# Optimization experiments

Hardware: AMD Instinct MI355X
Metric: run time of the kernel (lower is better)

Reference implementation:

```python
import jax, jax.numpy as jnp
import numpy as np

N, E = 10000, 320000
IN_D, HID, OUT_D, EIN, KH = 128, 32, 128, 1, 32
BN_EPS = 1e-5  # torch BatchNorm1d default eps


def bn(x, g, b):
    # training-mode batch norm with biased variance (torch normalization semantics)
    m = jnp.mean(x, axis=0)
    v = jnp.mean((x - m) ** 2, axis=0)
    return g * (x - m) / jnp.sqrt(v + BN_EPS) + b


def setup_inputs() -> dict:
    key = jax.random.key(0)
    ks = jax.random.split(key, 8)

    def w(k, shape, s=0.05):
        return jax.random.normal(k, shape, dtype=jnp.float32) * s

    return {
        "H": jax.random.normal(ks[0], (N, IN_D), dtype=jnp.float32),
        "edge_attr": jax.random.normal(ks[1], (E, EIN), dtype=jnp.float32),
        "edges": jax.random.randint(ks[2], (2, E), 0, N),
        # linear1: input_dim -> hidden_dim
        "w1": w(ks[3], (HID, IN_D)), "b1": jnp.zeros((HID,), jnp.float32),
        # kernel MLP: edge_input_dim -> kernel_hidden -> (hidden+1)*hidden
        "kw1": w(ks[4], (KH, EIN)), "kb1": jnp.zeros((KH,), jnp.float32),
        "kw2": w(ks[5], ((HID + 1) * HID, KH)), "kb2": jnp.zeros(((HID + 1) * HID,), jnp.float32),
        # linear2: hidden -> output
        "w2": w(ks[6], (OUT_D, HID)), "b2": jnp.zeros((OUT_D,), jnp.float32),
        # batchnorm affine params
        "g_in": jnp.ones((IN_D,), jnp.float32), "beta_in": jnp.zeros((IN_D,), jnp.float32),
        "g_msg": jnp.ones((HID,), jnp.float32), "beta_msg": jnp.zeros((HID,), jnp.float32),
        "g_upd": jnp.ones((HID,), jnp.float32), "beta_upd": jnp.zeros((HID,), jnp.float32),
        "g_out": jnp.ones((OUT_D,), jnp.float32), "beta_out": jnp.zeros((OUT_D,), jnp.float32),
    }


def reference(H, edge_attr, edges, w1, b1, kw1, kb1, kw2, kb2, w2, b2,
              g_in, beta_in, g_msg, beta_msg, g_upd, beta_upd, g_out, beta_out):
    node_out, node_in = edges[0], edges[1]

    Hn = bn(H, g_in, beta_in)                    # input_batch_norm
    layer_input = jax.nn.relu(Hn)                # dropout -> identity (eval)

    # message: gather -> linear1 -> BN -> relu
    msg = layer_input[node_in] @ w1.T + b1       # [E, HID]
    msg = jax.nn.relu(bn(msg, g_msg, beta_msg))

    # edge-conditioned dynamic kernel: [E, HID+1, HID]
    kern = jax.nn.relu(edge_attr @ kw1.T + kb1) @ kw2.T + kb2
    kern = kern.reshape(E, HID + 1, HID)
    # per-edge matvec + per-edge bias row
    msg = jnp.einsum('ejk,ek->ej', kern[:, 1:, :], msg) + kern[:, 0, :]

    # aggregate: scatter_add into nodes
    upd = jax.ops.segment_sum(msg, node_out, num_segments=N)
    upd = jax.nn.relu(bn(upd, g_upd, beta_upd))

    out = upd @ w2.T + b2                        # linear2
    return bn(out, g_out, beta_out)              # output_batch_norm
```

## Files before the change

### kernel.cpp

```cpp
#include <hip/hip_runtime.h>
#include <math.h>

constexpr int N_    = 10000;
constexpr int E_    = 320000;
constexpr int IND   = 128;
constexpr int HID   = 32;
constexpr int OUTD  = 128;
constexpr int NIV   = 33;
constexpr float EPS = 1e-5f;

constexpr size_t OFF_SUMH = 0;
constexpr size_t OFF_SQH  = 128;
constexpr size_t OFF_SUMP = 256;
constexpr size_t OFF_SQP  = 288;
constexpr size_t OFF_SUMU = 320;
constexpr size_t OFF_SQU  = 352;
constexpr size_t OFF_SUMO = 384;
constexpr size_t OFF_SQO  = 512;
constexpr size_t OFF_OCC  = 640;
constexpr size_t OFF_DEG  = 704;
constexpr size_t OFF_UPD  = 10752;
constexpr size_t ZERO_CNT = OFF_UPD + (size_t)N_*HID;
constexpr size_t OFF_BPS  = ZERO_CNT;
constexpr size_t OFF_M    = OFF_BPS + 32;
constexpr size_t OFF_C1   = 330816;
constexpr size_t OFF_C0   = OFF_C1 + (size_t)NIV*1056;
constexpr size_t OFF_P    = OFF_C0 + (size_t)NIV*1056;
constexpr size_t OFF_Q    = OFF_P + (size_t)N_*HID;
constexpr size_t OFF_IDX  = OFF_Q + (size_t)N_*HID;
constexpr size_t OFF_Y    = OFF_IDX + (size_t)E_;

__global__ __launch_bounds__(128)
void k_intervals(const float* __restrict__ kw1, const float* __restrict__ kb1,
                 const float* __restrict__ kw2, const float* __restrict__ kb2,
                 float* __restrict__ ws) {
    __shared__ float sel1[32], sel0[32];
    int* wsi = (int*)ws;
    int i = blockIdx.x;
    if (threadIdx.x == 0) {
        float bp[32]; int m = 0;
        for (int t = 0; t < 32; ++t) {
            float w = kw1[t];
            if (w != 0.f) bp[m++] = -kb1[t] / w;
        }
        for (int a = 1; a < m; ++a) {
            float v = bp[a]; int b = a - 1;
            while (b >= 0 && bp[b] > v) { bp[b+1] = bp[b]; --b; }
            bp[b+1] = v;
        }
        if (i == 0) {
            for (int k = 0; k < 32; ++k) ws[OFF_BPS + k] = (k < m) ? bp[k] : 0.f;
            wsi[OFF_M] = m;
        }
        float arep;
        if (m == 0 || i > m) arep = 0.f;
        else if (i == 0)     arep = bp[0]   - (1.f + 0.5f*fabsf(bp[0]));
        else if (i == m)     arep = bp[m-1] + (1.f + 0.5f*fabsf(bp[m-1]));
        else                 arep = (bp[i-1] < bp[i]) ? 0.5f*(bp[i-1] + bp[i]) : bp[i-1];
        for (int t = 0; t < 32; ++t) {
            bool s = (arep * kw1[t] + kb1[t]) > 0.f;
            sel1[t] = s ? kw1[t] : 0.f;
            sel0[t] = s ? kb1[t] : 0.f;
        }
    }
    __syncthreads();
    for (int r = threadIdx.x; r < 1056; r += blockDim.x) {
        float a1 = 0.f, a0 = 0.f;
        for (int t = 0; t < 32; ++t) {
            float w = kw2[r*32 + t];
            a1 += w * sel1[t];
            a0 += w * sel0[t];
        }
        ws[OFF_C1 + (size_t)i*1056 + r] = a1;
        ws[OFF_C0 + (size_t)i*1056 + r] = a0 + kb2[r];
    }
}

__global__ __launch_bounds__(256)
void k_stats_H(const float* __restrict__ H, float* __restrict__ ws) {
    __shared__ float shS[256], shQ[256];
    int t = threadIdx.x;
    int col = t & 127, half = t >> 7;
    float s = 0.f, q = 0.f;
    for (int r = blockIdx.x*2 + half; r < N_; r += gridDim.x*2) {
        float x = H[(size_t)r*IND + col];
        s += x; q += x*x;
    }
    shS[t] = s; shQ[t] = q;
    __syncthreads();
    if (t < 128) {
        atomicAdd(&ws[OFF_SUMH + t], shS[t] + shS[t+128]);
        atomicAdd(&ws[OFF_SQH  + t], shQ[t] + shQ[t+128]);
    }
}

__global__ __launch_bounds__(256)
void k_edge_idx(const float* __restrict__ ea, const int* __restrict__ edges,
                float* __restrict__ ws) {
    __shared__ int locc[NIV];
    __shared__ float bps[32];
    __shared__ int sm;
    int* wsi = (int*)ws;
    int t = threadIdx.x;
    if (t < NIV) locc[t] = 0;
    if (t < 32)  bps[t] = ws[OFF_BPS + t];
    if (t == 0)  sm = wsi[OFF_M];
    __syncthreads();
    int m = sm;
    for (int e = blockIdx.x*blockDim.x + t; e < E_; e += gridDim.x*blockDim.x) {
        float a = ea[e];
        int cnt = 0;
        for (int k = 0; k < m; ++k) cnt += (bps[k] < a) ? 1 : 0;
        wsi[OFF_IDX + e] = cnt;
        atomicAdd(&locc[cnt], 1);
        atomicAdd(&wsi[OFF_DEG + edges[E_ + e]], 1);
    }
    __syncthreads();
    if (t < NIV && locc[t] > 0) atomicAdd(&wsi[OFF_OCC + t], locc[t]);
}

__global__ __launch_bounds__(256)
void k_nodeP(const float* __restrict__ H, const float* __restrict__ w1,
             const float* __restrict__ b1, const float* __restrict__ g_in,
             const float* __restrict__ beta_in, float* __restrict__ ws) {
    __shared__ float X[2][IND];
    __shared__ float shP[256];
    int t = threadIdx.x;
    int nh = t >> 7, c = t & 127;
    float mean = ws[OFF_SUMH + c] * (1.f/N_);
    float var  = ws[OFF_SQH  + c] * (1.f/N_) - mean*mean;
    float istd = 1.f / sqrtf(var + EPS);
    float gc = g_in[c] * istd, bc = beta_in[c] - mean * gc;
    int j = c & 31, qd = c >> 5;
    for (int base = blockIdx.x*2; base < N_; base += gridDim.x*2) {
        int n = base + nh;
        float x = H[(size_t)n*IND + c];
        X[nh][c] = fmaxf(gc*x + bc, 0.f);
        __syncthreads();
        float part = 0.f;
        const float* wrow = w1 + j*IND + qd*32;
        const float* xq   = &X[nh][qd*32];
        for (int k = 0; k < 32; ++k) part += wrow[k] * xq[k];
        shP[t] = part;
        __syncthreads();
        if (c < 32) {
            float p = shP[nh*128 + j] + shP[nh*128 + j + 32]
                    + shP[nh*128 + j + 64] + shP[nh*128 + j + 96] + b1[j];
            ws[OFF_P + (size_t)n*HID + j] = p;
        }
        __syncthreads();
    }
}

__global__ __launch_bounds__(256)
void k_msg_stats(float* __restrict__ ws) {
    __shared__ float shS[256], shQ[256];
    const int* wsi = (const int*)ws;
    int t = threadIdx.x, j = t & 31, cp = t >> 5;
    float s = 0.f, q = 0.f;
    for (int n = blockIdx.x*8 + cp; n < N_; n += gridDim.x*8) {
        float w = (float)wsi[OFF_DEG + n];
        float p = ws[OFF_P + (size_t)n*HID + j];
        s += w*p; q += w*p*p;
    }
    shS[t] = s; shQ[t] = q;
    __syncthreads();
    if (t < 32) {
        float S = 0.f, Qq = 0.f;
        for (int c = 0; c < 8; ++c) { S += shS[t + 32*c]; Qq += shQ[t + 32*c]; }
        atomicAdd(&ws[OFF_SUMP + t], S);
        atomicAdd(&ws[OFF_SQP  + t], Qq);
    }
}

__global__ __launch_bounds__(256)
void k_Qy(const float* __restrict__ g_msg, const float* __restrict__ beta_msg,
          float* __restrict__ ws, int max_slots) {
    __shared__ float QL[8][HID];
    __shared__ int inv_slot[NIV];
    __shared__ int nslot;
    const int* wsi = (const int*)ws;
    int t = threadIdx.x, ln = t >> 5, j = t & 31;
    if (t == 0) {
        int ns = 0;
        for (int i = 0; i < NIV; ++i)
            if (wsi[OFF_OCC + i] > 0 && ns < max_slots) inv_slot[ns++] = i;
        nslot = ns;
    }
    __syncthreads();
    int ns = nslot;
    float mP = ws[OFF_SUMP + j] * (1.f/E_);
    float vP = ws[OFF_SQP  + j] * (1.f/E_) - mP*mP;
    float istd = 1.f / sqrtf(vP + EPS);
    float gc = g_msg[j]*istd, bc = beta_msg[j] - mP*gc;
    float2* yy = (float2*)(ws + OFF_Y);
    for (int base = blockIdx.x*8; base < N_; base += gridDim.x*8) {
        int n = base + ln;
        float p = ws[OFF_P + (size_t)n*HID + j];
        float qv = fmaxf(gc*p + bc, 0.f);
        ws[OFF_Q + (size_t)n*HID + j] = qv;
        QL[ln][j] = qv;
        __syncthreads();
        for (int s = 0; s < ns; ++s) {
            int i = inv_slot[s];
            const float* C1r = ws + OFF_C1 + (size_t)i*1056;
            const float* C0r = ws + OFF_C0 + (size_t)i*1056;
            float a1 = 0.f, a0 = 0.f;
            const float* ql = QL[ln];
            for (int k = 0; k < 32; ++k) {
                float qk = ql[k];
                a1 += C1r[32 + j*32 + k] * qk;
                a0 += C0r[32 + j*32 + k] * qk;
            }
            yy[((size_t)s*N_ + n)*32 + j] = make_float2(a1 + C1r[j], a0 + C0r[j]);
        }
        __syncthreads();
    }
}

__global__ __launch_bounds__(256)
void k_edge(const float* __restrict__ ea, const int* __restrict__ edges,
            float* __restrict__ ws, int max_slots) {
    __shared__ int slotL[NIV];
    const int* wsi = (const int*)ws;
    int t = threadIdx.x;
    if (t == 0) {
        int ns = 0;
        for (int i = 0; i < NIV; ++i) {
            if (wsi[OFF_OCC + i] > 0 && ns < max_slots) slotL[i] = ns++;
            else slotL[i] = -1;
        }
    }
    __syncthreads();
    long long g = (long long)blockIdx.x*blockDim.x + t;
    if (g >= (long long)E_*32) return;
    int e = (int)(g >> 5), j = (int)(g & 31);
    float a = ea[e];
    int i   = wsi[OFF_IDX + e];
    int s   = slotL[i];
    int nin = edges[E_ + e], nout = edges[e];
    float r;
    if (s >= 0) {
        const float2* yy = (const float2*)(ws + OFF_Y);
        float2 v = yy[((size_t)s*N_ + nin)*32 + j];
        r = fmaf(a, v.x, v.y);
    } else {
        const float* C1r = ws + OFF_C1 + (size_t)i*1056;
        const float* C0r = ws + OFF_C0 + (size_t)i*1056;
        const float* Qn  = ws + OFF_Q + (size_t)nin*HID;
        float a1 = 0.f, a0 = 0.f;
        for (int k = 0; k < 32; ++k) {
            float qk = Qn[k];
            a1 += C1r[32 + j*32 + k] * qk;
            a0 += C0r[32 + j*32 + k] * qk;
        }
        r = a*(a1 + C1r[j]) + (a0 + C0r[j]);
    }
    atomicAdd(&ws[OFF_UPD + (size_t)nout*HID + j], r);
}

__global__ __launch_bounds__(256)
void k_upd_stats(float* __restrict__ ws) {
    __shared__ float shS[256], shQ[256];
    int t = threadIdx.x, j = t & 31, cp = t >> 5;
    float s = 0.f, q = 0.f;
    for (int n = blockIdx.x*8 + cp; n < N_; n += gridDim.x*8) {
        float u = ws[OFF_UPD + (size_t)n*HID + j];
        s += u; q += u*u;
    }
    shS[t] = s; shQ[t] = q;
    __syncthreads();
    if (t < 32) {
        float S = 0.f, Qq = 0.f;
        for (int c = 0; c < 8; ++c) { S += shS[t + 32*c]; Qq += shQ[t + 32*c]; }
        atomicAdd(&ws[OFF_SUMU + t], S);
        atomicAdd(&ws[OFF_SQU  + t], Qq);
    }
}

__global__ __launch_bounds__(256)
void k_out(const float* __restrict__ w2, const float* __restrict__ b2,
           const float* __restrict__ g_upd, const float* __restrict__ beta_upd,
           float* __restrict__ ws, float* __restrict__ out) {
    __shared__ float U[2][HID];
    __shared__ float shS[256], shQ[256];
    int t = threadIdx.x, nh = t >> 7, o = t & 127;
    float gc = 0.f, bc = 0.f;
    if (o < 32) {
        float m = ws[OFF_SUMU + o]*(1.f/N_);
        float v = ws[OFF_SQU  + o]*(1.f/N_) - m*m;
        float istd = 1.f/sqrtf(v + EPS);
        gc = g_upd[o]*istd; bc = beta_upd[o] - m*gc;
    }
    float w2r[32];
    for (int k = 0; k < 32; ++k) w2r[k] = w2[o*32 + k];
    float bo = b2[o];
    float sO = 0.f, qO = 0.f;
    for (int base = blockIdx.x*2; base < N_; base += gridDim.x*2) {
        int n = base + nh;
        if (o < 32) {
            float u = ws[OFF_UPD + (size_t)n*HID + o];
            U[nh][o] = fmaxf(gc*u + bc, 0.f);
        }
        __syncthreads();
        float v = bo;
        for (int k = 0; k < 32; ++k) v += w2r[k]*U[nh][k];
        out[(size_t)n*OUTD + o] = v;
        sO += v; qO += v*v;
        __syncthreads();
    }
    shS[t] = sO; shQ[t] = qO;
    __syncthreads();
    if (t < 128) {
        atomicAdd(&ws[OFF_SUMO + t], shS[t] + shS[t+128]);
        atomicAdd(&ws[OFF_SQO  + t], shQ[t] + shQ[t+128]);
    }
}

__global__ __launch_bounds__(256)
void k_norm(const float* __restrict__ g_out, const float* __restrict__ beta_out,
            const float* __restrict__ ws, float* __restrict__ out) {
    int g = blockIdx.x*blockDim.x + threadIdx.x;
    if (g >= N_*OUTD) return;
    int o = g & 127;
    float m = ws[OFF_SUMO + o]*(1.f/N_);
    float v = ws[OFF_SQO  + o]*(1.f/N_) - m*m;
    float istd = 1.f/sqrtf(v + EPS);
    out[g] = g_out[o]*istd*(out[g] - m) + beta_out[o];
}

extern "C" void kernel_launch(void* const* d_in, const int* in_sizes, int n_in,
                              void* d_out, int out_size, void* d_ws, size_t ws_size,
                              hipStream_t stream) {
    const float* H        = (const float*)d_in[0];
    const float* ea       = (const float*)d_in[1];
    const int*   edges    = (const int*)  d_in[2];
    const float* w1       = (const float*)d_in[3];
    const float* b1       = (const float*)d_in[4];
    const float* kw1      = (const float*)d_in[5];
    const float* kb1      = (const float*)d_in[6];
    const float* kw2      = (const float*)d_in[7];
    const float* kb2      = (const float*)d_in[8];
    const float* w2       = (const float*)d_in[9];
    const float* b2       = (const float*)d_in[10];
    const float* g_in     = (const float*)d_in[11];
    const float* beta_in  = (const float*)d_in[12];
    const float* g_msg    = (const float*)d_in[13];
    const float* beta_msg = (const float*)d_in[14];
    const float* g_upd    = (const float*)d_in[15];
    const float* beta_upd = (const float*)d_in[16];
    const float* g_out    = (const float*)d_in[17];
    const float* beta_out = (const float*)d_in[18];
    float* ws  = (float*)d_ws;
    float* out = (float*)d_out;

    int max_slots = 0;
    size_t avail = ws_size / 4;
    if (avail > OFF_Y) max_slots = (int)((avail - OFF_Y) / ((size_t)N_*2*HID));
    if (max_slots > NIV) max_slots = NIV;

    hipMemsetAsync(d_ws, 0, ZERO_CNT*sizeof(float), stream);
    hipLaunchKernelGGL(k_intervals, dim3(NIV), dim3(128), 0, stream, kw1, kb1, kw2, kb2, ws);
    hipLaunchKernelGGL(k_stats_H,  dim3(128),  dim3(256), 0, stream, H, ws);
    hipLaunchKernelGGL(k_edge_idx, dim3(313),  dim3(256), 0, stream, ea, edges, ws);
    hipLaunchKernelGGL(k_nodeP,    dim3(1250), dim3(256), 0, stream, H, w1, b1, g_in, beta_in, ws);
    hipLaunchKernelGGL(k_msg_stats,dim3(64),   dim3(256), 0, stream, ws);
    hipLaunchKernelGGL(k_Qy,       dim3(1250), dim3(256), 0, stream, g_msg, beta_msg, ws, max_slots);
    hipLaunchKernelGGL(k_edge,     dim3((E_*32)/256), dim3(256), 0, stream, ea, edges, ws, max_slots);
    hipLaunchKernelGGL(k_upd_stats,dim3(64),   dim3(256), 0, stream, ws);
    hipLaunchKernelGGL(k_out,      dim3(250),  dim3(256), 0, stream, w2, b2, g_upd, beta_upd, ws, out);
    hipLaunchKernelGGL(k_norm,     dim3((N_*OUTD+255)/256), dim3(256), 0, stream, g_out, beta_out, ws, out);
}
```

Before: 311.1 us.

## Replace atomic edge scatter with CSR-sorted per-node gather and fused kernels

Builds a CSR by destination node (degree count, prefix scan, atomic slot placement) and computes each node's aggregate with a per-warp gather, replacing the per-element float atomics into the update buffer. For the two most common kernel intervals it accumulates a-weighted and plain sums of the per-edge message vectors and applies the shared 32x32 matrices once per node. Many small kernels are merged into fewer launches with block-range dispatch, and the node projection is rewritten with w1 held in shared memory. The per-node loop is serial over edges and its length varies with degree, which causes load imbalance, and it adds a sort step that itself uses atomics.

```diff
diff --git a/kernel.cpp b/kernel.cpp
--- a/kernel.cpp
+++ b/kernel.cpp
@@ -9,266 +9,307 @@
 constexpr int NIV   = 33;
 constexpr float EPS = 1e-5f;
 
-constexpr size_t OFF_SUMH = 0;
-constexpr size_t OFF_SQH  = 128;
-constexpr size_t OFF_SUMP = 256;
-constexpr size_t OFF_SQP  = 288;
-constexpr size_t OFF_SUMU = 320;
-constexpr size_t OFF_SQU  = 352;
-constexpr size_t OFF_SUMO = 384;
-constexpr size_t OFF_SQO  = 512;
-constexpr size_t OFF_OCC  = 640;
-constexpr size_t OFF_DEG  = 704;
-constexpr size_t OFF_UPD  = 10752;
-constexpr size_t ZERO_CNT = OFF_UPD + (size_t)N_*HID;
-constexpr size_t OFF_BPS  = ZERO_CNT;
-constexpr size_t OFF_M    = OFF_BPS + 32;
-constexpr size_t OFF_C1   = 330816;
-constexpr size_t OFF_C0   = OFF_C1 + (size_t)NIV*1056;
-constexpr size_t OFF_P    = OFF_C0 + (size_t)NIV*1056;
-constexpr size_t OFF_Q    = OFF_P + (size_t)N_*HID;
-constexpr size_t OFF_IDX  = OFF_Q + (size_t)N_*HID;
-constexpr size_t OFF_Y    = OFF_IDX + (size_t)E_;
-
-__global__ __launch_bounds__(128)
-void k_intervals(const float* __restrict__ kw1, const float* __restrict__ kb1,
-                 const float* __restrict__ kw2, const float* __restrict__ kb2,
-                 float* __restrict__ ws) {
+constexpr size_t OFF_SUMH   = 0;
+constexpr size_t OFF_SQH    = 128;
+constexpr size_t OFF_SUMP   = 256;
+constexpr size_t OFF_SQP    = 288;
+constexpr size_t OFF_SUMU   = 320;
+constexpr size_t OFF_SQU    = 352;
+constexpr size_t OFF_SUMO   = 384;
+constexpr size_t OFF_SQO    = 512;
+constexpr size_t OFF_OCC    = 640;
+constexpr size_t OFF_DEGIN  = 704;
+constexpr size_t OFF_DEGOUT = 10704;
+constexpr size_t ZERO_CNT   = 20704;
+constexpr size_t OFF_STARTS = 20740;
+constexpr size_t OFF_CUR    = 30744;
+constexpr size_t OFF_C1     = 40744;
+constexpr size_t OFF_C0     = 75592;
+constexpr size_t OFF_P      = 110440;
+constexpr size_t OFF_UPD    = 430440;
+constexpr size_t OFF_SORT   = 750440;
+constexpr size_t OFF_IDX    = 1070440;
+
+__device__ inline int compute_bps(const float* kw1, const float* kb1, float* bp) {
+    int m = 0;
+    for (int k = 0; k < 32; ++k) {
+        float w = kw1[k];
+        if (w != 0.f) bp[m++] = -kb1[k] / w;
+    }
+    for (int a = 1; a < m; ++a) {
+        float v = bp[a]; int b = a - 1;
+        while (b >= 0 && bp[b] > v) { bp[b+1] = bp[b]; --b; }
+        bp[b+1] = v;
+    }
+    return m;
+}
+
+__global__ __launch_bounds__(256)
+void k_A(const float* __restrict__ H,
+         const float* __restrict__ ea, const int* __restrict__ edges,
+         const float* __restrict__ kw1, const float* __restrict__ kb1,
+         const float* __restrict__ kw2, const float* __restrict__ kb2,
+         float* __restrict__ ws) {
     __shared__ float sel1[32], sel0[32];
-    int* wsi = (int*)ws;
-    int i = blockIdx.x;
-    if (threadIdx.x == 0) {
-        float bp[32]; int m = 0;
-        for (int t = 0; t < 32; ++t) {
-            float w = kw1[t];
-            if (w != 0.f) bp[m++] = -kb1[t] / w;
-        }
-        for (int a = 1; a < m; ++a) {
-            float v = bp[a]; int b = a - 1;
-            while (b >= 0 && bp[b] > v) { bp[b+1] = bp[b]; --b; }
-            bp[b+1] = v;
-        }
-        if (i == 0) {
-            for (int k = 0; k < 32; ++k) ws[OFF_BPS + k] = (k < m) ? bp[k] : 0.f;
-            wsi[OFF_M] = m;
-        }
-        float arep;
-        if (m == 0 || i > m) arep = 0.f;
-        else if (i == 0)     arep = bp[0]   - (1.f + 0.5f*fabsf(bp[0]));
-        else if (i == m)     arep = bp[m-1] + (1.f + 0.5f*fabsf(bp[m-1]));
-        else                 arep = (bp[i-1] < bp[i]) ? 0.5f*(bp[i-1] + bp[i]) : bp[i-1];
-        for (int t = 0; t < 32; ++t) {
-            bool s = (arep * kw1[t] + kb1[t]) > 0.f;
-            sel1[t] = s ? kw1[t] : 0.f;
-            sel0[t] = s ? kb1[t] : 0.f;
-        }
-    }
-    __syncthreads();
-    for (int r = threadIdx.x; r < 1056; r += blockDim.x) {
-        float a1 = 0.f, a0 = 0.f;
-        for (int t = 0; t < 32; ++t) {
-            float w = kw2[r*32 + t];
-            a1 += w * sel1[t];
-            a0 += w * sel0[t];
-        }
-        ws[OFF_C1 + (size_t)i*1056 + r] = a1;
-        ws[OFF_C0 + (size_t)i*1056 + r] = a0 + kb2[r];
-    }
-}
-
-__global__ __launch_bounds__(256)
-void k_stats_H(const float* __restrict__ H, float* __restrict__ ws) {
     __shared__ float shS[256], shQ[256];
-    int t = threadIdx.x;
-    int col = t & 127, half = t >> 7;
-    float s = 0.f, q = 0.f;
-    for (int r = blockIdx.x*2 + half; r < N_; r += gridDim.x*2) {
-        float x = H[(size_t)r*IND + col];
-        s += x; q += x*x;
-    }
-    shS[t] = s; shQ[t] = q;
-    __syncthreads();
-    if (t < 128) {
-        atomicAdd(&ws[OFF_SUMH + t], shS[t] + shS[t+128]);
-        atomicAdd(&ws[OFF_SQH  + t], shQ[t] + shQ[t+128]);
-    }
-}
-
-__global__ __launch_bounds__(256)
-void k_edge_idx(const float* __restrict__ ea, const int* __restrict__ edges,
-                float* __restrict__ ws) {
     __shared__ int locc[NIV];
     __shared__ float bps[32];
     __shared__ int sm;
     int* wsi = (int*)ws;
     int t = threadIdx.x;
-    if (t < NIV) locc[t] = 0;
-    if (t < 32)  bps[t] = ws[OFF_BPS + t];
-    if (t == 0)  sm = wsi[OFF_M];
-    __syncthreads();
-    int m = sm;
-    for (int e = blockIdx.x*blockDim.x + t; e < E_; e += gridDim.x*blockDim.x) {
-        float a = ea[e];
-        int cnt = 0;
-        for (int k = 0; k < m; ++k) cnt += (bps[k] < a) ? 1 : 0;
-        wsi[OFF_IDX + e] = cnt;
-        atomicAdd(&locc[cnt], 1);
-        atomicAdd(&wsi[OFF_DEG + edges[E_ + e]], 1);
-    }
-    __syncthreads();
-    if (t < NIV && locc[t] > 0) atomicAdd(&wsi[OFF_OCC + t], locc[t]);
-}
-
-__global__ __launch_bounds__(256)
-void k_nodeP(const float* __restrict__ H, const float* __restrict__ w1,
-             const float* __restrict__ b1, const float* __restrict__ g_in,
-             const float* __restrict__ beta_in, float* __restrict__ ws) {
-    __shared__ float X[2][IND];
-    __shared__ float shP[256];
+    int bid = blockIdx.x;
+
+    if (bid < 33) {
+        int i = bid;
+        if (t == 0) {
+            float bp[32];
+            int m = compute_bps(kw1, kb1, bp);
+            float arep;
+            if (m == 0 || i > m) arep = 0.f;
+            else if (i == 0)     arep = bp[0]   - (1.f + 0.5f*fabsf(bp[0]));
+            else if (i == m)     arep = bp[m-1] + (1.f + 0.5f*fabsf(bp[m-1]));
+            else                 arep = (bp[i-1] < bp[i]) ? 0.5f*(bp[i-1] + bp[i]) : bp[i-1];
+            for (int k = 0; k < 32; ++k) {
+                bool s = (arep * kw1[k] + kb1[k]) > 0.f;
+                sel1[k] = s ? kw1[k] : 0.f;
+                sel0[k] = s ? kb1[k] : 0.f;
+            }
+        }
+        __syncthreads();
+        for (int r = t; r < 1056; r += 256) {
+            float a1 = 0.f, a0 = 0.f;
+            for (int k = 0; k < 32; ++k) {
+                float w = kw2[r*32 + k];
+                a1 += w * sel1[k];
+                a0 += w * sel0[k];
+            }
+            ws[OFF_C1 + (size_t)i*1056 + r] = a1;
+            ws[OFF_C0 + (size_t)i*1056 + r] = a0 + kb2[r];
+        }
+    } else if (bid < 161) {
+        int b2 = bid - 33;
+        int col = t & 127, half = t >> 7;
+        float s = 0.f, q = 0.f;
+        for (int r = b2*2 + half; r < N_; r += 128*2) {
+            float x = H[(size_t)r*IND + col];
+            s += x; q += x*x;
+        }
+        shS[t] = s; shQ[t] = q;
+        __syncthreads();
+        if (t < 128) {
+            atomicAdd(&ws[OFF_SUMH + t], shS[t] + shS[t+128]);
+            atomicAdd(&ws[OFF_SQH  + t], shQ[t] + shQ[t+128]);
+        }
+    } else {
+        int b2 = bid - 161;
+        if (t < NIV) locc[t] = 0;
+        if (t == 0) {
+            float bp[32];
+            int m = compute_bps(kw1, kb1, bp);
+            for (int k = 0; k < 32; ++k) bps[k] = (k < m) ? bp[k] : 0.f;
+            sm = m;
+        }
+        __syncthreads();
+        int m = sm;
+        for (int e = b2*256 + t; e < E_; e += 313*256) {
+            float a = ea[e];
+            int cnt = 0;
+            for (int k = 0; k < m; ++k) cnt += (bps[k] < a) ? 1 : 0;
+            wsi[OFF_IDX + e] = cnt;
+            atomicAdd(&locc[cnt], 1);
+            atomicAdd(&wsi[OFF_DEGIN  + edges[E_ + e]], 1);
+            atomicAdd(&wsi[OFF_DEGOUT + edges[e]],      1);
+        }
+        __syncthreads();
+        if (t < NIV && locc[t] > 0) atomicAdd(&wsi[OFF_OCC + t], locc[t]);
+    }
+}
+
+__global__ __launch_bounds__(256)
+void k_B(const float* __restrict__ H, const float* __restrict__ w1,
+         const float* __restrict__ b1, const float* __restrict__ g_in,
+         const float* __restrict__ beta_in, float* __restrict__ ws) {
+    __shared__ float w1L[32*129];
+    __shared__ float xl[8][128];
+    __shared__ int part[256];
+    int* wsi = (int*)ws;
     int t = threadIdx.x;
-    int nh = t >> 7, c = t & 127;
-    float mean = ws[OFF_SUMH + c] * (1.f/N_);
-    float var  = ws[OFF_SQH  + c] * (1.f/N_) - mean*mean;
-    float istd = 1.f / sqrtf(var + EPS);
-    float gc = g_in[c] * istd, bc = beta_in[c] - mean * gc;
-    int j = c & 31, qd = c >> 5;
-    for (int base = blockIdx.x*2; base < N_; base += gridDim.x*2) {
-        int n = base + nh;
-        float x = H[(size_t)n*IND + c];
-        X[nh][c] = fmaxf(gc*x + bc, 0.f);
-        __syncthreads();
-        float part = 0.f;
-        const float* wrow = w1 + j*IND + qd*32;
-        const float* xq   = &X[nh][qd*32];
-        for (int k = 0; k < 32; ++k) part += wrow[k] * xq[k];
-        shP[t] = part;
-        __syncthreads();
-        if (c < 32) {
-            float p = shP[nh*128 + j] + shP[nh*128 + j + 32]
-                    + shP[nh*128 + j + 64] + shP[nh*128 + j + 96] + b1[j];
-            ws[OFF_P + (size_t)n*HID + j] = p;
-        }
-        __syncthreads();
-    }
-}
-
-__global__ __launch_bounds__(256)
-void k_msg_stats(float* __restrict__ ws) {
+
+    if (blockIdx.x == 0) {
+        int base = t * 40;
+        int loc[40];
+        int s = 0;
+        for (int i = 0; i < 40; ++i) {
+            int idx = base + i;
+            int v = (idx < N_) ? wsi[OFF_DEGOUT + idx] : 0;
+            loc[i] = s; s += v;
+        }
+        part[t] = s;
+        __syncthreads();
+        for (int off = 1; off < 256; off <<= 1) {
+            int add = (t >= off) ? part[t - off] : 0;
+            __syncthreads();
+            part[t] += add;
+            __syncthreads();
+        }
+        int pre = (t > 0) ? part[t-1] : 0;
+        for (int i = 0; i < 40; ++i) {
+            int idx = base + i;
+            if (idx <= N_) {
+                int v = pre + loc[i];
+                wsi[OFF_STARTS + idx] = v;
+                if (idx < N_) wsi[OFF_CUR + idx] = v;
+            }
+        }
+        return;
+    }
+
+    int g = t >> 5, j = t & 31;
+    for (int idx = t; idx < 4096; idx += 256)
+        w1L[(idx >> 7)*129 + (idx & 127)] = w1[idx];
+
+    int n = (blockIdx.x - 1)*8 + g;
+    float4 h4 = ((const float4*)(H + (size_t)n*IND))[j];
+    float4 m4 = ((const float4*)(ws + OFF_SUMH))[j];
+    float4 q4 = ((const float4*)(ws + OFF_SQH))[j];
+    float4 gg = ((const float4*)g_in)[j];
+    float4 bb = ((const float4*)beta_in)[j];
+    float4 xv;
+    {
+        float* hp = (float*)&h4; float* mp = (float*)&m4; float* qp = (float*)&q4;
+        float* gp = (float*)&gg; float* bp = (float*)&bb; float* xp = (float*)&xv;
+        for (int i = 0; i < 4; ++i) {
+            float mean = mp[i] * (1.f/N_);
+            float var  = qp[i] * (1.f/N_) - mean*mean;
+            float istd = 1.f / sqrtf(var + EPS);
+            float gc = gp[i]*istd, bc = bp[i] - mean*gc;
+            xp[i] = fmaxf(fmaf(gc, hp[i], bc), 0.f);
+        }
+    }
+    ((float4*)&xl[g][0])[j] = xv;
+    __syncthreads();
+    float p = b1[j];
+    const float* wr = &w1L[j*129];
+    const float* xr = &xl[g][0];
+    #pragma unroll 8
+    for (int k = 0; k < 128; ++k) p = fmaf(wr[k], xr[k], p);
+    ws[OFF_P + (size_t)n*HID + j] = p;
+}
+
+__global__ __launch_bounds__(256)
+void k_C(const int* __restrict__ edges, float* __restrict__ ws) {
     __shared__ float shS[256], shQ[256];
-    const int* wsi = (const int*)ws;
-    int t = threadIdx.x, j = t & 31, cp = t >> 5;
-    float s = 0.f, q = 0.f;
-    for (int n = blockIdx.x*8 + cp; n < N_; n += gridDim.x*8) {
-        float w = (float)wsi[OFF_DEG + n];
-        float p = ws[OFF_P + (size_t)n*HID + j];
-        s += w*p; q += w*p*p;
-    }
-    shS[t] = s; shQ[t] = q;
-    __syncthreads();
+    int* wsi = (int*)ws;
+    int t = threadIdx.x;
+    if (blockIdx.x < 313) {
+        int b2 = blockIdx.x;
+        for (int e = b2*256 + t; e < E_; e += 313*256) {
+            int nout = edges[e];
+            int pos = atomicAdd(&wsi[OFF_CUR + nout], 1);
+            wsi[OFF_SORT + pos] = e;
+        }
+    } else {
+        int b2 = blockIdx.x - 313;
+        int j = t & 31, cp = t >> 5;
+        float s = 0.f, q = 0.f;
+        for (int n = b2*8 + cp; n < N_; n += 64*8) {
+            float w = (float)wsi[OFF_DEGIN + n];
+            float p = ws[OFF_P + (size_t)n*HID + j];
+            s += w*p; q += w*p*p;
+        }
+        shS[t] = s; shQ[t] = q;
+        __syncthreads();
+        if (t < 32) {
+            float S = 0.f, Qq = 0.f;
+            for (int c = 0; c < 8; ++c) { S += shS[t + 32*c]; Qq += shQ[t + 32*c]; }
+            atomicAdd(&ws[OFF_SUMP + t], S);
+            atomicAdd(&ws[OFF_SQP  + t], Qq);
+        }
+    }
+}
+
+__global__ __launch_bounds__(256)
+void k_D(const float* __restrict__ ea, const int* __restrict__ edges,
+         const float* __restrict__ g_msg, const float* __restrict__ beta_msg,
+         float* __restrict__ ws) {
+    __shared__ float A[4][32*33];
+    __shared__ float Bv[4][32];
+    __shared__ float zl[8][4][32];
+    __shared__ float shS[256], shQ[256];
+    __shared__ int s_slot0, s_slot1;
+    int* wsi = (int*)ws;
+    int t = threadIdx.x, g = t >> 5, j = t & 31;
+
+    if (t == 0) {
+        int a0 = -1, a1 = -1;
+        for (int i = 0; i < NIV; ++i)
+            if (wsi[OFF_OCC + i] > 0) { if (a0 < 0) a0 = i; else if (a1 < 0) a1 = i; }
+        s_slot0 = a0; s_slot1 = a1;
+    }
+    __syncthreads();
+    int s0 = s_slot0, s1 = s_slot1;
+
+    for (int idx = t; idx < 1024; idx += 256) {
+        int jj = idx >> 5, kk = idx & 31;
+        A[0][jj*33+kk] = (s0 >= 0) ? ws[OFF_C1 + (size_t)s0*1056 + 32 + idx] : 0.f;
+        A[1][jj*33+kk] = (s0 >= 0) ? ws[OFF_C0 + (size_t)s0*1056 + 32 + idx] : 0.f;
+        A[2][jj*33+kk] = (s1 >= 0) ? ws[OFF_C1 + (size_t)s1*1056 + 32 + idx] : 0.f;
+        A[3][jj*33+kk] = (s1 >= 0) ? ws[OFF_C0 + (size_t)s1*1056 + 32 + idx] : 0.f;
+    }
     if (t < 32) {
-        float S = 0.f, Qq = 0.f;
-        for (int c = 0; c < 8; ++c) { S += shS[t + 32*c]; Qq += shQ[t + 32*c]; }
-        atomicAdd(&ws[OFF_SUMP + t], S);
-        atomicAdd(&ws[OFF_SQP  + t], Qq);
-    }
-}
-
-__global__ __launch_bounds__(256)
-void k_Qy(const float* __restrict__ g_msg, const float* __restrict__ beta_msg,
-          float* __restrict__ ws, int max_slots) {
-    __shared__ float QL[8][HID];
-    __shared__ int inv_slot[NIV];
-    __shared__ int nslot;
-    const int* wsi = (const int*)ws;
-    int t = threadIdx.x, ln = t >> 5, j = t & 31;
-    if (t == 0) {
-        int ns = 0;
-        for (int i = 0; i < NIV; ++i)
-            if (wsi[OFF_OCC + i] > 0 && ns < max_slots) inv_slot[ns++] = i;
-        nslot = ns;
-    }
-    __syncthreads();
-    int ns = nslot;
+        Bv[0][t] = (s0 >= 0) ? ws[OFF_C1 + (size_t)s0*1056 + t] : 0.f;
+        Bv[1][t] = (s0 >= 0) ? ws[OFF_C0 + (size_t)s0*1056 + t] : 0.f;
+        Bv[2][t] = (s1 >= 0) ? ws[OFF_C1 + (size_t)s1*1056 + t] : 0.f;
+        Bv[3][t] = (s1 >= 0) ? ws[OFF_C0 + (size_t)s1*1056 + t] : 0.f;
+    }
     float mP = ws[OFF_SUMP + j] * (1.f/E_);
     float vP = ws[OFF_SQP  + j] * (1.f/E_) - mP*mP;
     float istd = 1.f / sqrtf(vP + EPS);
     float gc = g_msg[j]*istd, bc = beta_msg[j] - mP*gc;
-    float2* yy = (float2*)(ws + OFF_Y);
-    for (int base = blockIdx.x*8; base < N_; base += gridDim.x*8) {
-        int n = base + ln;
-        float p = ws[OFF_P + (size_t)n*HID + j];
-        float qv = fmaxf(gc*p + bc, 0.f);
-        ws[OFF_Q + (size_t)n*HID + j] = qv;
-        QL[ln][j] = qv;
-        __syncthreads();
-        for (int s = 0; s < ns; ++s) {
-            int i = inv_slot[s];
-            const float* C1r = ws + OFF_C1 + (size_t)i*1056;
-            const float* C0r = ws + OFF_C0 + (size_t)i*1056;
-            float a1 = 0.f, a0 = 0.f;
-            const float* ql = QL[ln];
+    __syncthreads();
+
+    int n = blockIdx.x*8 + g;
+    int st = wsi[OFF_STARTS + n], en = wsi[OFF_STARTS + n + 1];
+    float za0 = 0.f, zb0 = 0.f, za1 = 0.f, zb1 = 0.f;
+    float suma0 = 0.f, suma1 = 0.f, rfall = 0.f;
+    int c0 = 0, c1 = 0;
+    for (int p = st; p < en; ++p) {
+        int e   = wsi[OFF_SORT + p];
+        float a = ea[e];
+        int iv  = wsi[OFF_IDX + e];
+        int nin = edges[E_ + e];
+        float pv = ws[OFF_P + (size_t)nin*HID + j];
+        float q  = fmaxf(fmaf(gc, pv, bc), 0.f);
+        if (iv == s0)      { za0 = fmaf(a, q, za0); zb0 += q; suma0 += a; ++c0; }
+        else if (iv == s1) { za1 = fmaf(a, q, za1); zb1 += q; suma1 += a; ++c1; }
+        else {
+            const float* C1r = ws + OFF_C1 + (size_t)iv*1056;
+            const float* C0r = ws + OFF_C0 + (size_t)iv*1056;
+            float d1 = 0.f, d0 = 0.f;
             for (int k = 0; k < 32; ++k) {
-                float qk = ql[k];
-                a1 += C1r[32 + j*32 + k] * qk;
-                a0 += C0r[32 + j*32 + k] * qk;
+                float qk = __shfl(q, k, 32);
+                d1 += C1r[32 + j*32 + k] * qk;
+                d0 += C0r[32 + j*32 + k] * qk;
             }
-            yy[((size_t)s*N_ + n)*32 + j] = make_float2(a1 + C1r[j], a0 + C0r[j]);
-        }
-        __syncthreads();
-    }
-}
-
-__global__ __launch_bounds__(256)
-void k_edge(const float* __restrict__ ea, const int* __restrict__ edges,
-            float* __restrict__ ws, int max_slots) {
-    __shared__ int slotL[NIV];
-    const int* wsi = (const int*)ws;
-    int t = threadIdx.x;
-    if (t == 0) {
-        int ns = 0;
-        for (int i = 0; i < NIV; ++i) {
-            if (wsi[OFF_OCC + i] > 0 && ns < max_slots) slotL[i] = ns++;
-            else slotL[i] = -1;
-        }
-    }
-    __syncthreads();
-    long long g = (long long)blockIdx.x*blockDim.x + t;
-    if (g >= (long long)E_*32) return;
-    int e = (int)(g >> 5), j = (int)(g & 31);
-    float a = ea[e];
-    int i   = wsi[OFF_IDX + e];
-    int s   = slotL[i];
-    int nin = edges[E_ + e], nout = edges[e];
-    float r;
-    if (s >= 0) {
-        const float2* yy = (const float2*)(ws + OFF_Y);
-        float2 v = yy[((size_t)s*N_ + nin)*32 + j];
-        r = fmaf(a, v.x, v.y);
-    } else {
-        const float* C1r = ws + OFF_C1 + (size_t)i*1056;
-        const float* C0r = ws + OFF_C0 + (size_t)i*1056;
-        const float* Qn  = ws + OFF_Q + (size_t)nin*HID;
-        float a1 = 0.f, a0 = 0.f;
-        for (int k = 0; k < 32; ++k) {
-            float qk = Qn[k];
-            a1 += C1r[32 + j*32 + k] * qk;
-            a0 += C0r[32 + j*32 + k] * qk;
-        }
-        r = a*(a1 + C1r[j]) + (a0 + C0r[j]);
-    }
-    atomicAdd(&ws[OFF_UPD + (size_t)nout*HID + j], r);
-}
-
-__global__ __launch_bounds__(256)
-void k_upd_stats(float* __restrict__ ws) {
-    __shared__ float shS[256], shQ[256];
-    int t = threadIdx.x, j = t & 31, cp = t >> 5;
-    float s = 0.f, q = 0.f;
-    for (int n = blockIdx.x*8 + cp; n < N_; n += gridDim.x*8) {
-        float u = ws[OFF_UPD + (size_t)n*HID + j];
-        s += u; q += u*u;
-    }
-    shS[t] = s; shQ[t] = q;
+            rfall += a*(d1 + C1r[j]) + (d0 + C0r[j]);
+        }
+    }
+    zl[g][0][j] = za0; zl[g][1][j] = zb0; zl[g][2][j] = za1; zl[g][3][j] = zb1;
+    __syncthreads();
+
+    float acc = rfall;
+    if (s0 >= 0) acc += suma0*Bv[0][j] + (float)c0*Bv[1][j];
+    if (s1 >= 0) acc += suma1*Bv[2][j] + (float)c1*Bv[3][j];
+    const float* z0 = zl[g][0]; const float* z1 = zl[g][1];
+    const float* z2 = zl[g][2]; const float* z3 = zl[g][3];
+    #pragma unroll 4
+    for (int k = 0; k < 32; ++k) {
+        acc += A[0][j*33+k]*z0[k] + A[1][j*33+k]*z1[k]
+             + A[2][j*33+k]*z2[k] + A[3][j*33+k]*z3[k];
+    }
+    ws[OFF_UPD + (size_t)n*HID + j] = acc;
+
+    shS[t] = acc; shQ[t] = acc*acc;
     __syncthreads();
     if (t < 32) {
         float S = 0.f, Qq = 0.f;
@@ -279,9 +320,9 @@
 }
 
 __global__ __launch_bounds__(256)
-void k_out(const float* __restrict__ w2, const float* __restrict__ b2,
-           const float* __restrict__ g_upd, const float* __restrict__ beta_upd,
-           float* __restrict__ ws, float* __restrict__ out) {
+void k_F(const float* __restrict__ w2, const float* __restrict__ b2,
+         const float* __restrict__ g_upd, const float* __restrict__ beta_upd,
+         float* __restrict__ ws, float* __restrict__ out) {
     __shared__ float U[2][HID];
     __shared__ float shS[256], shQ[256];
     int t = threadIdx.x, nh = t >> 7, o = t & 127;
@@ -300,11 +341,11 @@
         int n = base + nh;
         if (o < 32) {
             float u = ws[OFF_UPD + (size_t)n*HID + o];
-            U[nh][o] = fmaxf(gc*u + bc, 0.f);
+            U[nh][o] = fmaxf(fmaf(gc, u, bc), 0.f);
         }
         __syncthreads();
         float v = bo;
-        for (int k = 0; k < 32; ++k) v += w2r[k]*U[nh][k];
+        for (int k = 0; k < 32; ++k) v = fmaf(w2r[k], U[nh][k], v);
         out[(size_t)n*OUTD + o] = v;
         sO += v; qO += v*v;
         __syncthreads();
@@ -318,8 +359,8 @@
 }
 
 __global__ __launch_bounds__(256)
-void k_norm(const float* __restrict__ g_out, const float* __restrict__ beta_out,
-            const float* __restrict__ ws, float* __restrict__ out) {
+void k_G(const float* __restrict__ g_out, const float* __restrict__ beta_out,
+         const float* __restrict__ ws, float* __restrict__ out) {
     int g = blockIdx.x*blockDim.x + threadIdx.x;
     if (g >= N_*OUTD) return;
     int o = g & 127;
@@ -354,20 +395,11 @@
     float* ws  = (float*)d_ws;
     float* out = (float*)d_out;
 
-    int max_slots = 0;
-    size_t avail = ws_size / 4;
-    if (avail > OFF_Y) max_slots = (int)((avail - OFF_Y) / ((size_t)N_*2*HID));
-    if (max_slots > NIV) max_slots = NIV;
-
     hipMemsetAsync(d_ws, 0, ZERO_CNT*sizeof(float), stream);
-    hipLaunchKernelGGL(k_intervals, dim3(NIV), dim3(128), 0, stream, kw1, kb1, kw2, kb2, ws);
-    hipLaunchKernelGGL(k_stats_H,  dim3(128),  dim3(256), 0, stream, H, ws);
-    hipLaunchKernelGGL(k_edge_idx, dim3(313),  dim3(256), 0, stream, ea, edges, ws);
-    hipLaunchKernelGGL(k_nodeP,    dim3(1250), dim3(256), 0, stream, H, w1, b1, g_in, beta_in, ws);
-    hipLaunchKernelGGL(k_msg_stats,dim3(64),   dim3(256), 0, stream, ws);
-    hipLaunchKernelGGL(k_Qy,       dim3(1250), dim3(256), 0, stream, g_msg, beta_msg, ws, max_slots);
-    hipLaunchKernelGGL(k_edge,     dim3((E_*32)/256), dim3(256), 0, stream, ea, edges, ws, max_slots);
-    hipLaunchKernelGGL(k_upd_stats,dim3(64),   dim3(256), 0, stream, ws);
-    hipLaunchKernelGGL(k_out,      dim3(250),  dim3(256), 0, stream, w2, b2, g_upd, beta_upd, ws, out);
-    hipLaunchKernelGGL(k_norm,     dim3((N_*OUTD+255)/256), dim3(256), 0, stream, g_out, beta_out, ws, out);
-}
+    hipLaunchKernelGGL(k_A, dim3(474),  dim3(256), 0, stream, H, ea, edges, kw1, kb1, kw2, kb2, ws);
+    hipLaunchKernelGGL(k_B, dim3(1251), dim3(256), 0, stream, H, w1, b1, g_in, beta_in, ws);
+    hipLaunchKernelGGL(k_C, dim3(377),  dim3(256), 0, stream, edges, ws);
+    hipLaunchKernelGGL(k_D, dim3(1250), dim3(256), 0, stream, ea, edges, g_msg, beta_msg, ws);
+    hipLaunchKernelGGL(k_F, dim3(250),  dim3(256), 0, stream, w2, b2, g_upd, beta_upd, ws, out);
+    hipLaunchKernelGGL(k_G, dim3((N_*OUTD + 255)/256), dim3(256), 0, stream, g_out, beta_out, ws, out);
+}
```

Result: faster. 298.2 us (-4.2%).
